# Kernel optimization log

Hardware: AMD Instinct MI355X
Metric: run time of the kernel (lower is better)

## Reference

```python
import jax, jax.numpy as jnp
import numpy as np

B, L, K, G, C, S = 1024, 32, 8, 8, 128, 32
D_IN = 2 * L + K + S  # masked z (L) + mask (L) + target (K) + shared (S)
TAU = 1.0
EPS = 1e-5
NEG_INF = -1e9  # stands in for torch's -9e15 diagonal fill; sigmoid(-1e9)=0


def setup_inputs() -> dict:
    key = jax.random.key(0)
    ks = jax.random.split(key, 24)
    eye = jnp.eye(K, dtype=bool)
    kaiming = lambda k, shape: jax.random.uniform(k, shape, jnp.float32, -1.0, 1.0) * np.sqrt(6.0 / shape[-1])
    return {
        "z_sample": jax.random.normal(ks[0], (B, L), jnp.float32),
        "target": jax.random.randint(ks[1], (B,), 0, K),
        "z_mean": jax.random.normal(ks[2], (B, L), jnp.float32),
        "z_logstd": 0.1 * jax.random.normal(ks[3], (B, L), jnp.float32),
        "z_shared": jax.random.normal(ks[4], (B, S), jnp.float32),
        "u_gumbel": jax.random.uniform(ks[5], (B, L, K), jnp.float32),
        "u_adj": jax.random.uniform(ks[6], (B, G, K, K), jnp.float32),
        "target_params": 0.1 * jax.random.normal(ks[7], (L, K), jnp.float32),
        "enco_theta": jnp.where(eye, NEG_INF, jax.random.normal(ks[8], (K, K), jnp.float32)),
        "enco_gamma": jnp.where(eye, NEG_INF, jax.random.normal(ks[9], (K, K), jnp.float32)),
        "W1": kaiming(ks[10], (L, C, D_IN)),
        "b1": jnp.zeros((L, C), jnp.float32),
        "gn1_w": jnp.ones((L, C), jnp.float32),
        "gn1_b": jnp.zeros((L, C), jnp.float32),
        "W2": kaiming(ks[11], (L, C, C)),
        "b2": jnp.zeros((L, C), jnp.float32),
        "gn2_w": jnp.ones((L, C), jnp.float32),
        "gn2_b": jnp.zeros((L, C), jnp.float32),
        "W3": 0.01 * jax.random.normal(ks[12], (L, 2, C), jnp.float32),
        "b3": jnp.zeros((L, 2), jnp.float32),
        "tanh_scale": jnp.zeros((L, 2), jnp.float32),
    }


def _mv_linear(x, W, b):
    # x: [B,G,L,d_in], W: [L,d_out,d_in] -> [B,G,L,d_out]  (per-latent independent linear)
    return jnp.einsum("bgld,lhd->bglh", x, W) + b


def _mv_groupnorm(x, w, b):
    # GroupNorm(L groups over L*C channels) == per-(sample, latent) normalization over C
    mu = x.mean(-1, keepdims=True)
    var = ((x - mu) ** 2).mean(-1, keepdims=True)
    return (x - mu) * jax.lax.rsqrt(var + EPS) * w + b


def reference(z_sample, target, z_mean, z_logstd, z_shared, u_gumbel, u_adj,
              target_params, enco_theta, enco_gamma,
              W1, b1, gn1_w, gn1_b, W2, b2, gn2_w, gn2_b, W3, b3, tanh_scale):
    dt = z_sample.dtype
    target_oh = jax.nn.one_hot(target, K, dtype=dt)  # [B,K]

    # hard gumbel-softmax with straight-through estimator: psi assigns latents to causal vars
    g = -jnp.log(-jnp.log(u_gumbel + 1e-10) + 1e-10)
    soft = jax.nn.softmax((target_params[None] + g) / TAU, axis=-1)  # [B,L,K]
    hard = jax.nn.one_hot(jnp.argmax(soft, axis=-1), K, dtype=dt)
    psi = hard + soft - jax.lax.stop_gradient(soft)  # [B,L,K]

    # ENCO graph sampling: edge prob = sigmoid(theta)*sigmoid(gamma), Bernoulli samples
    edge_prob = jax.nn.sigmoid(enco_theta) * jax.nn.sigmoid(enco_gamma)  # [K,K]
    adj = (u_adj < edge_prob[None, None]).astype(dt)  # [B,G,K,K], adj[k,l]=1: k->l

    # latent-level parent mask: mask[b,g,i,j]=1 iff latent j is a parent of latent i
    latent_mask = jnp.einsum("bil,bgkl,bjk->bgij", psi, adj, psi)  # [B,G,L,L]
    latent_mask = latent_mask * (1.0 - jnp.eye(L, dtype=dt))

    # per-latent network input: [masked parents, mask, intervention indicator, shared]
    z_masked = latent_mask * z_sample[:, None, None, :]                        # [B,G,L,L]
    t_inp = jnp.broadcast_to((psi * target_oh[:, None, :])[:, None], (B, G, L, K))
    zs = jnp.broadcast_to(z_shared[:, None, None, :], (B, G, L, S))
    s_inp = jnp.concatenate([z_masked, latent_mask, t_inp, zs], axis=-1)       # [B,G,L,D_IN]

    h = jax.nn.silu(_mv_groupnorm(_mv_linear(s_inp, W1, b1), gn1_w, gn1_b))
    h = jax.nn.silu(_mv_groupnorm(_mv_linear(h, W2, b2), gn2_w, gn2_b))
    h = _mv_linear(h, W3, b3)                                                  # [B,G,L,2]
    sc = jnp.exp(tanh_scale)                                                   # [L,2]
    h = jnp.tanh(h / sc) * sc                                                  # MultivarStableTanh
    prior_mean, prior_logstd = h[..., 0], h[..., 1]                            # [B,G,L]

    # KL(q(z) || p(z)) per latent, averaged over graph samples, summed over latents
    var_q = jnp.exp(2.0 * z_logstd)[:, None]                                   # [B,1,L]
    kld = (prior_logstd - z_logstd[:, None]
           + (var_q + (z_mean[:, None] - prior_mean) ** 2) / (2.0 * jnp.exp(2.0 * prior_logstd))
           - 0.5)                                                              # [B,G,L]
    return kld.mean(axis=1).sum(axis=-1)                                       # [B]
```

## Files before the change

kernel.cpp:

```cpp
#include <hip/hip_runtime.h>
#include <hip/hip_bf16.h>

#define B_DIM 1024
#define L_DIM 32
#define K_DIM 8
#define G_DIM 8
#define C_DIM 128
#define S_DIM 32
#define DIN   104

typedef __bf16  bf16x8 __attribute__((ext_vector_type(8)));
typedef float   f32x4  __attribute__((ext_vector_type(4)));
typedef float   f32x2  __attribute__((ext_vector_type(2)));

union frag_u { uint4 u; bf16x8 v; };

static __device__ __forceinline__ unsigned int pk2(float a, float b) {
    __hip_bfloat162 h = __float22bfloat162_rn(make_float2(a, b));
    union { __hip_bfloat162 h; unsigned int u; } v; v.h = h; return v.u;
}
static __device__ __forceinline__ unsigned int pk2v(f32x2 a) { return pk2(a.x, a.y); }
static __device__ __forceinline__ bf16x8 ld_frag(const unsigned short* p) {
    frag_u t; t.u = *(const uint4*)p; return t.v;
}

#define LOG2E 1.44269504f

__global__ __launch_bounds__(256) void prep_kernel(
    const float* __restrict__ u_gumbel,
    const float* __restrict__ u_adj,
    const float* __restrict__ target_params,
    const float* __restrict__ enco_theta,
    const float* __restrict__ enco_gamma,
    const int*   __restrict__ target,
    const float* __restrict__ W1,
    const float* __restrict__ W2,
    float*       __restrict__ out,
    unsigned char* __restrict__ cvarpk,
    unsigned int*  __restrict__ wsmask,
    unsigned short* __restrict__ wscr)
{
    const int t = threadIdx.x;
    if (blockIdx.x >= 1024) {
        int gtid  = (blockIdx.x - 1024) * 256 + t;
        int lane  = gtid & 63;
        int ks    = (gtid >> 6) & 3;
        int mt    = (gtid >> 8) & 3;
        int wm    = (gtid >> 10) & 1;
        int l     = (gtid >> 11) & 31;
        int which = gtid >> 16;
        int m  = 16 * (4 * wm + mt) + (lane & 15);
        int k0 = ks * 32 + (lane >> 4) * 8;
        uint4 o;
        if (which == 0) {
            if (k0 >= 104) {
                o = make_uint4(0u, 0u, 0u, 0u);
            } else {
                const float* p = W1 + (size_t)l * 13312 + m * 104 + k0;
                float4 a = *(const float4*)p, bq = *(const float4*)(p + 4);
                o = make_uint4(pk2(a.x, a.y), pk2(a.z, a.w), pk2(bq.x, bq.y), pk2(bq.z, bq.w));
            }
        } else {
            const float* p = W2 + (size_t)l * 16384 + m * 128 + k0;
            float4 a = *(const float4*)p, bq = *(const float4*)(p + 4);
            o = make_uint4(pk2(a.x, a.y), pk2(a.z, a.w), pk2(bq.x, bq.y), pk2(bq.z, bq.w));
        }
        *(uint4*)(wscr + (size_t)gtid * 8) = o;
        return;
    }

    __shared__ double ep[64];
    __shared__ unsigned char cv8[32];
    __shared__ unsigned long long adjb[8];
    const int b = blockIdx.x;
    if (t < 64) {
        double th = (double)enco_theta[t];
        double ga = (double)enco_gamma[t];
        ep[t] = (1.0 / (1.0 + exp(-th))) * (1.0 / (1.0 + exp(-ga)));
    }
    if (t == 0) out[b] = 0.0f;
    __syncthreads();

    {
        const int l = t >> 3, k = t & 7;
        float uf = u_gumbel[b * 256 + t];
        float gf = -__logf(-__logf(uf + 1e-10f) + 1e-10f);
        float vf = target_params[t] + gf;
        float vm = vf; int bk = k;
        #pragma unroll
        for (int off = 1; off < 8; off <<= 1) {
            float ov = __shfl_xor(vm, off, 64);
            int  obk = __shfl_xor(bk, off, 64);
            if (ov > vm || (ov == vm && obk < bk)) { vm = ov; bk = obk; }
        }
        int amb = ((k != bk) && (vm - vf < 1e-3f)) ? 1 : 0;
        #pragma unroll
        for (int off = 1; off < 8; off <<= 1) amb |= __shfl_xor(amb, off, 64);
        if (amb) {
            double ud = (double)uf;
            double gd = -log(-log(ud + 1e-10) + 1e-10);
            double vd = (double)target_params[t] + gd;
            int bk2 = k;
            #pragma unroll
            for (int off = 1; off < 8; off <<= 1) {
                double ov = __shfl_xor(vd, off, 64);
                int   obk = __shfl_xor(bk2, off, 64);
                if (ov > vd || (ov == vd && obk < bk2)) { vd = ov; bk2 = obk; }
            }
            bk = bk2;
        }
        if (k == 0) {
            int tg = target[b];
            unsigned char pkd = (unsigned char)(bk | ((bk == tg) ? 8 : 0));
            cvarpk[b * 32 + l] = pkd;
            cv8[l] = pkd;
        }
    }
    {
        const int wv = t >> 6, lane = t & 63;
        #pragma unroll
        for (int q = 0; q < 2; ++q) {
            int gg = wv + 4 * q;
            double u = (double)u_adj[b * 512 + gg * 64 + lane];
            unsigned long long m = __ballot(u < ep[lane]);
            if (lane == 0) adjb[gg] = m;
        }
    }
    __syncthreads();

    {
        const int g = t >> 5, l = t & 31;
        int lam = cv8[l] & 7;
        unsigned long long bits = adjb[g] >> lam;
        unsigned int mask = 0u;
        #pragma unroll
        for (int j = 0; j < 32; ++j) {
            int kap = cv8[j] & 7;
            mask |= ((unsigned int)(bits >> (kap * 8)) & 1u) << j;
        }
        mask &= ~(1u << l);
        wsmask[l * 8192 + b * 8 + g] = mask;
    }
}

__global__ __launch_bounds__(256, 2) void fused_kernel(
    const float* __restrict__ z_sample,
    const float* __restrict__ z_mean,
    const float* __restrict__ z_logstd,
    const float* __restrict__ z_shared,
    const float* __restrict__ pb1,
    const float* __restrict__ g1w,
    const float* __restrict__ g1b,
    const float* __restrict__ pb2,
    const float* __restrict__ g2w,
    const float* __restrict__ g2b,
    const float* __restrict__ W3,
    const float* __restrict__ pb3,
    const float* __restrict__ tsc,
    const unsigned short* __restrict__ wscr,
    const unsigned char*  __restrict__ cvarpk,
    const unsigned int*   __restrict__ wsmask,
    float* __restrict__ out)
{
    __shared__ __align__(16) unsigned short XH[4][32][136];
    __shared__ float p_g1w[128], p_g1b[128], p_b1[128];
    __shared__ float p_g2w[128], p_g2b[128], p_b2[128];
    __shared__ float p_w3[2][128];
    __shared__ float p_b3[2], p_ts[2];
    __shared__ unsigned int  msk[128];
    __shared__ unsigned char cvl[16];

    const int tid  = threadIdx.x;
    const int w    = tid >> 6, lane = tid & 63;
    const int lo   = lane & 15, hi = lane >> 4;
    const int l    = blockIdx.x & 31;
    const int grp  = blockIdx.x >> 5;

    if (tid < 128) {
        int c = tid;
        p_g1w[c] = g1w[l * 128 + c];  p_g1b[c] = g1b[l * 128 + c];
        p_b1[c]  = pb1[l * 128 + c];  p_w3[0][c] = W3[l * 256 + c];
        msk[c]   = wsmask[l * 8192 + grp * 128 + c];
    } else {
        int c = tid - 128;
        p_g2w[c] = g2w[l * 128 + c];  p_g2b[c] = g2b[l * 128 + c];
        p_b2[c]  = pb2[l * 128 + c];  p_w3[1][c] = W3[l * 256 + 128 + c];
    }
    if (tid < 16) cvl[tid] = cvarpk[(size_t)(grp * 16 + tid) * 32 + l];
    if (tid == 0) {
        p_b3[0] = pb3[l * 2];  p_b3[1] = pb3[l * 2 + 1];
        p_ts[0] = tsc[l * 2];  p_ts[1] = tsc[l * 2 + 1];
    }
    __syncthreads();

    #pragma unroll
    for (int nt = 0; nt < 2; ++nt) {
        int r  = nt * 16 + lo;
        int bl = (w * 32 + r) >> 3;
        int bg = grp * 16 + bl;
        unsigned int m32 = msk[w * 32 + r];
        unsigned int mq  = (m32 >> (hi * 8)) & 0xffu;
        const float4* zp = (const float4*)(z_sample + bg * 32 + hi * 8);
        float4 za = zp[0], zb = zp[1];
        uint4 f0;
        f0.x = pk2((mq & 1u)   ? za.x : 0.f, (mq & 2u)   ? za.y : 0.f);
        f0.y = pk2((mq & 4u)   ? za.z : 0.f, (mq & 8u)   ? za.w : 0.f);
        f0.z = pk2((mq & 16u)  ? zb.x : 0.f, (mq & 32u)  ? zb.y : 0.f);
        f0.w = pk2((mq & 64u)  ? zb.z : 0.f, (mq & 128u) ? zb.w : 0.f);
        uint4 f1;
        f1.x = ((mq & 1u)   ? 0x3F80u : 0u) | ((mq & 2u)   ? 0x3F800000u : 0u);
        f1.y = ((mq & 4u)   ? 0x3F80u : 0u) | ((mq & 8u)   ? 0x3F800000u : 0u);
        f1.z = ((mq & 16u)  ? 0x3F80u : 0u) | ((mq & 32u)  ? 0x3F800000u : 0u);
        f1.w = ((mq & 64u)  ? 0x3F80u : 0u) | ((mq & 128u) ? 0x3F800000u : 0u);
        unsigned int cb8 = cvl[bl];
        int lam = cb8 & 7, tf = (cb8 >> 3) & 1;
        int zsb = (hi == 0) ? 24 : (hi - 1) * 8;
        const float4* sp = (const float4*)(z_shared + bg * 32 + zsb);
        float4 sa = sp[0], sb = sp[1];
        uint4 fz;
        fz.x = pk2(sa.x, sa.y); fz.y = pk2(sa.z, sa.w);
        fz.z = pk2(sb.x, sb.y); fz.w = pk2(sb.z, sb.w);
        unsigned int ohw = tf ? (0x3F80u << ((lam & 1) << 4)) : 0u;
        int lq = lam >> 1;
        uint4 fo;
        fo.x = (lq == 0) ? ohw : 0u;
        fo.y = (lq == 1) ? ohw : 0u;
        fo.z = (lq == 2) ? ohw : 0u;
        fo.w = (lq == 3) ? ohw : 0u;
        bool h0 = (hi == 0);
        uint4 f2, f3;
        f2.x = h0 ? fo.x : fz.x;  f2.y = h0 ? fo.y : fz.y;
        f2.z = h0 ? fo.z : fz.z;  f2.w = h0 ? fo.w : fz.w;
        f3.x = h0 ? fz.x : 0u;    f3.y = h0 ? fz.y : 0u;
        f3.z = h0 ? fz.z : 0u;    f3.w = h0 ? fz.w : 0u;
        *(uint4*)&XH[w][r][hi * 8]      = f0;
        *(uint4*)&XH[w][r][32 + hi * 8] = f1;
        *(uint4*)&XH[w][r][64 + hi * 8] = f2;
        *(uint4*)&XH[w][r][96 + hi * 8] = f3;
    }

    const float inv128 = 1.0f / 128.0f;
    const unsigned short* w1p = wscr + (size_t)(l * 32) * 512 + lane * 8;
    const unsigned short* w2p = wscr + (size_t)((32 + l) * 32) * 512 + lane * 8;

    f32x4 acc[8][2];
    #pragma unroll
    for (int cb = 0; cb < 8; ++cb)
        #pragma unroll
        for (int nt = 0; nt < 2; ++nt) acc[cb][nt] = (f32x4){0.f, 0.f, 0.f, 0.f};
    {
        bf16x8 wfA[2], wfB[2];
        wfA[0] = ld_frag(w1p + 0 * 512);
        wfA[1] = ld_frag(w1p + 4 * 512);
        #pragma unroll
        for (int ks = 0; ks < 4; ++ks) {
            bf16x8 bf0 = ld_frag(&XH[w][lo][ks * 32 + hi * 8]);
            bf16x8 bf1 = ld_frag(&XH[w][16 + lo][ks * 32 + hi * 8]);
            #pragma unroll
            for (int p = 0; p < 4; ++p) {
                int ncb = (p < 3) ? (2 * p + 2) : 0;
                int nks = (p < 3) ? ks : ks + 1;
                if (p < 3 || ks < 3) {
                    wfB[0] = ld_frag(w1p + (ncb * 4 + nks) * 512);
                    wfB[1] = ld_frag(w1p + ((ncb + 1) * 4 + nks) * 512);
                }
                int cb = 2 * p;
                acc[cb][0]     = __builtin_amdgcn_mfma_f32_16x16x32_bf16(wfA[0], bf0, acc[cb][0], 0, 0, 0);
                acc[cb][1]     = __builtin_amdgcn_mfma_f32_16x16x32_bf16(wfA[0], bf1, acc[cb][1], 0, 0, 0);
                acc[cb + 1][0] = __builtin_amdgcn_mfma_f32_16x16x32_bf16(wfA[1], bf0, acc[cb + 1][0], 0, 0, 0);
                acc[cb + 1][1] = __builtin_amdgcn_mfma_f32_16x16x32_bf16(wfA[1], bf1, acc[cb + 1][1], 0, 0, 0);
                wfA[0] = wfB[0];  wfA[1] = wfB[1];
            }
        }
    }

    f32x2 s1v[2] = {(f32x2){0.f, 0.f}, (f32x2){0.f, 0.f}};
    f32x2 s2v[2] = {(f32x2){0.f, 0.f}, (f32x2){0.f, 0.f}};
    #pragma unroll
    for (int cb = 0; cb < 8; ++cb) {
        f32x2 bLo = *(const f32x2*)&p_b1[cb * 16 + hi * 4];
        f32x2 bHi = *(const f32x2*)&p_b1[cb * 16 + hi * 4 + 2];
        #pragma unroll
        for (int nt = 0; nt < 2; ++nt) {
            f32x2 vLo = (f32x2){acc[cb][nt][0], acc[cb][nt][1]} + bLo;
            f32x2 vHi = (f32x2){acc[cb][nt][2], acc[cb][nt][3]} + bHi;
            acc[cb][nt][0] = vLo.x;  acc[cb][nt][1] = vLo.y;
            acc[cb][nt][2] = vHi.x;  acc[cb][nt][3] = vHi.y;
            s1v[nt] += vLo + vHi;
            s2v[nt] += vLo * vLo + vHi * vHi;
        }
    }
    float rstd[2], nrm_off[2];
    #pragma unroll
    for (int nt = 0; nt < 2; ++nt) {
        float s1 = s1v[nt].x + s1v[nt].y;
        float s2 = s2v[nt].x + s2v[nt].y;
        s1 += __shfl_xor(s1, 16, 64);  s1 += __shfl_xor(s1, 32, 64);
        s2 += __shfl_xor(s2, 16, 64);  s2 += __shfl_xor(s2, 32, 64);
        float m_  = s1 * inv128;
        float var = s2 * inv128 - m_ * m_;
        float r   = rsqrtf(var + 1e-5f);
        rstd[nt] = r;  nrm_off[nt] = -m_ * r;
    }
    #pragma unroll
    for (int cb = 0; cb < 8; ++cb) {
        f32x2 gwLo = *(const f32x2*)&p_g1w[cb * 16 + hi * 4];
        f32x2 gwHi = *(const f32x2*)&p_g1w[cb * 16 + hi * 4 + 2];
        f32x2 gbLo = *(const f32x2*)&p_g1b[cb * 16 + hi * 4];
        f32x2 gbHi = *(const f32x2*)&p_g1b[cb * 16 + hi * 4 + 2];
        #pragma unroll
        for (int nt = 0; nt < 2; ++nt) {
            f32x2 rr  = (f32x2){rstd[nt], rstd[nt]};
            f32x2 oo  = (f32x2){nrm_off[nt], nrm_off[nt]};
            f32x2 vLo = (f32x2){acc[cb][nt][0], acc[cb][nt][1]};
            f32x2 vHi = (f32x2){acc[cb][nt][2], acc[cb][nt][3]};
            f32x2 xLo = (vLo * rr + oo) * gwLo + gbLo;
            f32x2 xHi = (vHi * rr + oo) * gwHi + gbHi;
            f32x2 aLo = xLo * (f32x2){-LOG2E, -LOG2E};
            f32x2 aHi = xHi * (f32x2){-LOG2E, -LOG2E};
            f32x2 eLo = (f32x2){__builtin_amdgcn_exp2f(aLo.x), __builtin_amdgcn_exp2f(aLo.y)};
            f32x2 eHi = (f32x2){__builtin_amdgcn_exp2f(aHi.x), __builtin_amdgcn_exp2f(aHi.y)};
            f32x2 dLo = eLo + (f32x2){1.f, 1.f};
            f32x2 dHi = eHi + (f32x2){1.f, 1.f};
            f32x2 yLo = xLo * (f32x2){__builtin_amdgcn_rcpf(dLo.x), __builtin_amdgcn_rcpf(dLo.y)};
            f32x2 yHi = xHi * (f32x2){__builtin_amdgcn_rcpf(dHi.x), __builtin_amdgcn_rcpf(dHi.y)};
            *(uint2*)&XH[w][nt * 16 + lo][cb * 16 + hi * 4] =
                make_uint2(pk2v(yLo), pk2v(yHi));
        }
    }

    #pragma unroll
    for (int cb = 0; cb < 8; ++cb)
        #pragma unroll
        for (int nt = 0; nt < 2; ++nt) acc[cb][nt] = (f32x4){0.f, 0.f, 0.f, 0.f};
    {
        bf16x8 wfA[2], wfB[2];
        wfA[0] = ld_frag(w2p + 0 * 512);
        wfA[1] = ld_frag(w2p + 4 * 512);
        #pragma unroll
        for (int ks = 0; ks < 4; ++ks) {
            bf16x8 bf0 = ld_frag(&XH[w][lo][ks * 32 + hi * 8]);
            bf16x8 bf1 = ld_frag(&XH[w][16 + lo][ks * 32 + hi * 8]);
            #pragma unroll
            for (int p = 0; p < 4; ++p) {
                int ncb = (p < 3) ? (2 * p + 2) : 0;
                int nks = (p < 3) ? ks : ks + 1;
                if (p < 3 || ks < 3) {
                    wfB[0] = ld_frag(w2p + (ncb * 4 + nks) * 512);
                    wfB[1] = ld_frag(w2p + ((ncb + 1) * 4 + nks) * 512);
                }
                int cb = 2 * p;
                acc[cb][0]     = __builtin_amdgcn_mfma_f32_16x16x32_bf16(wfA[0], bf0, acc[cb][0], 0, 0, 0);
                acc[cb][1]     = __builtin_amdgcn_mfma_f32_16x16x32_bf16(wfA[0], bf1, acc[cb][1], 0, 0, 0);
                acc[cb + 1][0] = __builtin_amdgcn_mfma_f32_16x16x32_bf16(wfA[1], bf0, acc[cb + 1][0], 0, 0, 0);
                acc[cb + 1][1] = __builtin_amdgcn_mfma_f32_16x16x32_bf16(wfA[1], bf1, acc[cb + 1][1], 0, 0, 0);
                wfA[0] = wfB[0];  wfA[1] = wfB[1];
            }
        }
    }

    f32x2 t1v[2] = {(f32x2){0.f, 0.f}, (f32x2){0.f, 0.f}};
    f32x2 t2v[2] = {(f32x2){0.f, 0.f}, (f32x2){0.f, 0.f}};
    #pragma unroll
    for (int cb = 0; cb < 8; ++cb) {
        f32x2 bLo = *(const f32x2*)&p_b2[cb * 16 + hi * 4];
        f32x2 bHi = *(const f32x2*)&p_b2[cb * 16 + hi * 4 + 2];
        #pragma unroll
        for (int nt = 0; nt < 2; ++nt) {
            f32x2 vLo = (f32x2){acc[cb][nt][0], acc[cb][nt][1]} + bLo;
            f32x2 vHi = (f32x2){acc[cb][nt][2], acc[cb][nt][3]} + bHi;
            acc[cb][nt][0] = vLo.x;  acc[cb][nt][1] = vLo.y;
            acc[cb][nt][2] = vHi.x;  acc[cb][nt][3] = vHi.y;
            t1v[nt] += vLo + vHi;
            t2v[nt] += vLo * vLo + vHi * vHi;
        }
    }
    float rstd2[2], off2[2];
    #pragma unroll
    for (int nt = 0; nt < 2; ++nt) {
        float s1 = t1v[nt].x + t1v[nt].y;
        float s2 = t2v[nt].x + t2v[nt].y;
        s1 += __shfl_xor(s1, 16, 64);  s1 += __shfl_xor(s1, 32, 64);
        s2 += __shfl_xor(s2, 16, 64);  s2 += __shfl_xor(s2, 32, 64);
        float m_  = s1 * inv128;
        float var = s2 * inv128 - m_ * m_;
        float r   = rsqrtf(var + 1e-5f);
        rstd2[nt] = r;  off2[nt] = -m_ * r;
    }
    f32x2 pm2[2] = {(f32x2){0.f, 0.f}, (f32x2){0.f, 0.f}};
    f32x2 pl2[2] = {(f32x2){0.f, 0.f}, (f32x2){0.f, 0.f}};
    #pragma unroll
    for (int cb = 0; cb < 8; ++cb) {
        f32x2 gwLo = *(const f32x2*)&p_g2w[cb * 16 + hi * 4];
        f32x2 gwHi = *(const f32x2*)&p_g2w[cb * 16 + hi * 4 + 2];
        f32x2 gbLo = *(const f32x2*)&p_g2b[cb * 16 + hi * 4];
        f32x2 gbHi = *(const f32x2*)&p_g2b[cb * 16 + hi * 4 + 2];
        f32x2 w0Lo = *(const f32x2*)&p_w3[0][cb * 16 + hi * 4];
        f32x2 w0Hi = *(const f32x2*)&p_w3[0][cb * 16 + hi * 4 + 2];
        f32x2 w1Lo = *(const f32x2*)&p_w3[1][cb * 16 + hi * 4];
        f32x2 w1Hi = *(const f32x2*)&p_w3[1][cb * 16 + hi * 4 + 2];
        #pragma unroll
        for (int nt = 0; nt < 2; ++nt) {
            f32x2 rr  = (f32x2){rstd2[nt], rstd2[nt]};
            f32x2 oo  = (f32x2){off2[nt], off2[nt]};
            f32x2 vLo = (f32x2){acc[cb][nt][0], acc[cb][nt][1]};
            f32x2 vHi = (f32x2){acc[cb][nt][2], acc[cb][nt][3]};
            f32x2 xLo = (vLo * rr + oo) * gwLo + gbLo;
            f32x2 xHi = (vHi * rr + oo) * gwHi + gbHi;
            f32x2 aLo = xLo * (f32x2){-LOG2E, -LOG2E};
            f32x2 aHi = xHi * (f32x2){-LOG2E, -LOG2E};
            f32x2 eLo = (f32x2){__builtin_amdgcn_exp2f(aLo.x), __builtin_amdgcn_exp2f(aLo.y)};
            f32x2 eHi = (f32x2){__builtin_amdgcn_exp2f(aHi.x), __builtin_amdgcn_exp2f(aHi.y)};
            f32x2 dLo = eLo + (f32x2){1.f, 1.f};
            f32x2 dHi = eHi + (f32x2){1.f, 1.f};
            f32x2 yLo = xLo * (f32x2){__builtin_amdgcn_rcpf(dLo.x), __builtin_amdgcn_rcpf(dLo.y)};
            f32x2 yHi = xHi * (f32x2){__builtin_amdgcn_rcpf(dHi.x), __builtin_amdgcn_rcpf(dHi.y)};
            pm2[nt] += yLo * w0Lo + yHi * w0Hi;
            pl2[nt] += yLo * w1Lo + yHi * w1Hi;
        }
    }

    {
        float sc0 = __expf(p_ts[0]), sc1 = __expf(p_ts[1]);
        float is0 = __expf(-p_ts[0]), is1 = __expf(-p_ts[1]);
        #pragma unroll
        for (int nt = 0; nt < 2; ++nt) {
            int r  = w * 32 + nt * 16 + lo;
            int bg = grp * 16 + (r >> 3);
            float zm = z_mean[bg * 32 + l];
            float zl = z_logstd[bg * 32 + l];
            float pmp = pm2[nt].x + pm2[nt].y;
            float plp = pl2[nt].x + pl2[nt].y;
            pmp += __shfl_xor(pmp, 16, 64);  pmp += __shfl_xor(pmp, 32, 64);
            plp += __shfl_xor(plp, 16, 64);  plp += __shfl_xor(plp, 32, 64);
            float pm = pmp + p_b3[0];
            float pl = plp + p_b3[1];
            float e0 = __expf(2.0f * pm * is0);
            pm = (1.0f - 2.0f * __fdividef(1.0f, e0 + 1.0f)) * sc0;
            float e1 = __expf(2.0f * pl * is1);
            pl = (1.0f - 2.0f * __fdividef(1.0f, e1 + 1.0f)) * sc1;
            float vq = __expf(2.0f * zl);
            float d  = zm - pm;
            float kld = pl - zl + (vq + d * d) * 0.5f * __expf(-2.0f * pl) - 0.5f;
            kld += __shfl_xor(kld, 1, 64);
            kld += __shfl_xor(kld, 2, 64);
            kld += __shfl_xor(kld, 4, 64);
            if (hi == 0 && (lo & 7) == 0) atomicAdd(&out[bg], kld * 0.125f);
        }
    }
}

extern "C" void kernel_launch(void* const* d_in, const int* in_sizes, int n_in,
                              void* d_out, int out_size, void* d_ws, size_t ws_size,
                              hipStream_t stream) {
    const float* z_sample      = (const float*)d_in[0];
    const int*   target        = (const int*)d_in[1];
    const float* z_mean        = (const float*)d_in[2];
    const float* z_logstd      = (const float*)d_in[3];
    const float* z_shared      = (const float*)d_in[4];
    const float* u_gumbel      = (const float*)d_in[5];
    const float* u_adj         = (const float*)d_in[6];
    const float* target_params = (const float*)d_in[7];
    const float* enco_theta    = (const float*)d_in[8];
    const float* enco_gamma    = (const float*)d_in[9];
    const float* W1            = (const float*)d_in[10];
    const float* pb1           = (const float*)d_in[11];
    const float* g1w           = (const float*)d_in[12];
    const float* g1b           = (const float*)d_in[13];
    const float* W2            = (const float*)d_in[14];
    const float* pb2           = (const float*)d_in[15];
    const float* g2w           = (const float*)d_in[16];
    const float* g2b           = (const float*)d_in[17];
    const float* W3            = (const float*)d_in[18];
    const float* pb3           = (const float*)d_in[19];
    const float* tsc           = (const float*)d_in[20];

    unsigned char* cvarpk = (unsigned char*)d_ws;
    unsigned int*  wsmask = (unsigned int*)((char*)d_ws + 32768);
    unsigned short* wscr  = (unsigned short*)((char*)d_ws + 32768 + 1048576);

    prep_kernel<<<1536, 256, 0, stream>>>(u_gumbel, u_adj, target_params,
                                          enco_theta, enco_gamma, target,
                                          W1, W2, (float*)d_out,
                                          cvarpk, wsmask, wscr);
    fused_kernel<<<2048, 256, 0, stream>>>(z_sample, z_mean, z_logstd, z_shared,
                                           pb1, g1w, g1b, pb2, g2w, g2b,
                                           W3, pb3, tsc, wscr, cvarpk, wsmask,
                                           (float*)d_out);
}
```

Before: 156.9 us.

## Split fused kernel into single-wave blocks and drop block barrier

Changes the fused kernel from 4-wave blocks to 1-wave blocks with 4x more blocks, each handling 4 batch rows for one latent. Each block now loads its own per-latent norm/bias parameters, removing the __syncthreads and shrinking LDS per block. This trades extra redundant parameter loads for finer-grained scheduling and no barrier.

```diff
diff --git a/kernel.cpp b/kernel.cpp
--- a/kernel.cpp
+++ b/kernel.cpp
@@ -143,7 +143,7 @@
     }
 }
 
-__global__ __launch_bounds__(256, 2) void fused_kernel(
+__global__ __launch_bounds__(64, 2) void fused_kernel(
     const float* __restrict__ z_sample,
     const float* __restrict__ z_mean,
     const float* __restrict__ z_logstd,
@@ -162,43 +162,40 @@
     const unsigned int*   __restrict__ wsmask,
     float* __restrict__ out)
 {
-    __shared__ __align__(16) unsigned short XH[4][32][136];
+    __shared__ __align__(16) unsigned short XH[32][136];
     __shared__ float p_g1w[128], p_g1b[128], p_b1[128];
     __shared__ float p_g2w[128], p_g2b[128], p_b2[128];
     __shared__ float p_w3[2][128];
     __shared__ float p_b3[2], p_ts[2];
-    __shared__ unsigned int  msk[128];
-    __shared__ unsigned char cvl[16];
-
-    const int tid  = threadIdx.x;
-    const int w    = tid >> 6, lane = tid & 63;
+    __shared__ unsigned int  msk[32];
+    __shared__ unsigned char cvl[4];
+
+    const int lane = threadIdx.x & 63;
     const int lo   = lane & 15, hi = lane >> 4;
     const int l    = blockIdx.x & 31;
     const int grp  = blockIdx.x >> 5;
 
-    if (tid < 128) {
-        int c = tid;
+    #pragma unroll
+    for (int j = 0; j < 2; ++j) {
+        int c = lane + j * 64;
         p_g1w[c] = g1w[l * 128 + c];  p_g1b[c] = g1b[l * 128 + c];
         p_b1[c]  = pb1[l * 128 + c];  p_w3[0][c] = W3[l * 256 + c];
-        msk[c]   = wsmask[l * 8192 + grp * 128 + c];
-    } else {
-        int c = tid - 128;
         p_g2w[c] = g2w[l * 128 + c];  p_g2b[c] = g2b[l * 128 + c];
         p_b2[c]  = pb2[l * 128 + c];  p_w3[1][c] = W3[l * 256 + 128 + c];
     }
-    if (tid < 16) cvl[tid] = cvarpk[(size_t)(grp * 16 + tid) * 32 + l];
-    if (tid == 0) {
+    if (lane < 32) msk[lane] = wsmask[l * 8192 + grp * 32 + lane];
+    if (lane < 4)  cvl[lane] = cvarpk[(size_t)(grp * 4 + lane) * 32 + l];
+    if (lane == 0) {
         p_b3[0] = pb3[l * 2];  p_b3[1] = pb3[l * 2 + 1];
         p_ts[0] = tsc[l * 2];  p_ts[1] = tsc[l * 2 + 1];
     }
-    __syncthreads();
 
     #pragma unroll
     for (int nt = 0; nt < 2; ++nt) {
         int r  = nt * 16 + lo;
-        int bl = (w * 32 + r) >> 3;
-        int bg = grp * 16 + bl;
-        unsigned int m32 = msk[w * 32 + r];
+        int bl = r >> 3;
+        int bg = grp * 4 + bl;
+        unsigned int m32 = msk[r];
         unsigned int mq  = (m32 >> (hi * 8)) & 0xffu;
         const float4* zp = (const float4*)(z_sample + bg * 32 + hi * 8);
         float4 za = zp[0], zb = zp[1];
@@ -233,10 +230,10 @@
         f2.z = h0 ? fo.z : fz.z;  f2.w = h0 ? fo.w : fz.w;
         f3.x = h0 ? fz.x : 0u;    f3.y = h0 ? fz.y : 0u;
         f3.z = h0 ? fz.z : 0u;    f3.w = h0 ? fz.w : 0u;
-        *(uint4*)&XH[w][r][hi * 8]      = f0;
-        *(uint4*)&XH[w][r][32 + hi * 8] = f1;
-        *(uint4*)&XH[w][r][64 + hi * 8] = f2;
-        *(uint4*)&XH[w][r][96 + hi * 8] = f3;
+        *(uint4*)&XH[r][hi * 8]      = f0;
+        *(uint4*)&XH[r][32 + hi * 8] = f1;
+        *(uint4*)&XH[r][64 + hi * 8] = f2;
+        *(uint4*)&XH[r][96 + hi * 8] = f3;
     }
 
     const float inv128 = 1.0f / 128.0f;
@@ -254,8 +251,8 @@
         wfA[1] = ld_frag(w1p + 4 * 512);
         #pragma unroll
         for (int ks = 0; ks < 4; ++ks) {
-            bf16x8 bf0 = ld_frag(&XH[w][lo][ks * 32 + hi * 8]);
-            bf16x8 bf1 = ld_frag(&XH[w][16 + lo][ks * 32 + hi * 8]);
+            bf16x8 bf0 = ld_frag(&XH[lo][ks * 32 + hi * 8]);
+            bf16x8 bf1 = ld_frag(&XH[16 + lo][ks * 32 + hi * 8]);
             #pragma unroll
             for (int p = 0; p < 4; ++p) {
                 int ncb = (p < 3) ? (2 * p + 2) : 0;
@@ -324,7 +321,7 @@
             f32x2 dHi = eHi + (f32x2){1.f, 1.f};
             f32x2 yLo = xLo * (f32x2){__builtin_amdgcn_rcpf(dLo.x), __builtin_amdgcn_rcpf(dLo.y)};
             f32x2 yHi = xHi * (f32x2){__builtin_amdgcn_rcpf(dHi.x), __builtin_amdgcn_rcpf(dHi.y)};
-            *(uint2*)&XH[w][nt * 16 + lo][cb * 16 + hi * 4] =
+            *(uint2*)&XH[nt * 16 + lo][cb * 16 + hi * 4] =
                 make_uint2(pk2v(yLo), pk2v(yHi));
         }
     }
@@ -339,8 +336,8 @@
         wfA[1] = ld_frag(w2p + 4 * 512);
         #pragma unroll
         for (int ks = 0; ks < 4; ++ks) {
-            bf16x8 bf0 = ld_frag(&XH[w][lo][ks * 32 + hi * 8]);
-            bf16x8 bf1 = ld_frag(&XH[w][16 + lo][ks * 32 + hi * 8]);
+            bf16x8 bf0 = ld_frag(&XH[lo][ks * 32 + hi * 8]);
+            bf16x8 bf1 = ld_frag(&XH[16 + lo][ks * 32 + hi * 8]);
             #pragma unroll
             for (int p = 0; p < 4; ++p) {
                 int ncb = (p < 3) ? (2 * p + 2) : 0;
@@ -425,8 +422,8 @@
         float is0 = __expf(-p_ts[0]), is1 = __expf(-p_ts[1]);
         #pragma unroll
         for (int nt = 0; nt < 2; ++nt) {
-            int r  = w * 32 + nt * 16 + lo;
-            int bg = grp * 16 + (r >> 3);
+            int r  = nt * 16 + lo;
+            int bg = grp * 4 + (r >> 3);
             float zm = z_mean[bg * 32 + l];
             float zl = z_logstd[bg * 32 + l];
             float pmp = pm2[nt].x + pm2[nt].y;
@@ -483,8 +480,8 @@
                                           enco_theta, enco_gamma, target,
                                           W1, W2, (float*)d_out,
                                           cvarpk, wsmask, wscr);
-    fused_kernel<<<2048, 256, 0, stream>>>(z_sample, z_mean, z_logstd, z_shared,
-                                           pb1, g1w, g1b, pb2, g2w, g2b,
-                                           W3, pb3, tsc, wscr, cvarpk, wsmask,
-                                           (float*)d_out);
+    fused_kernel<<<8192, 64, 0, stream>>>(z_sample, z_mean, z_logstd, z_shared,
+                                          pb1, g1w, g1b, pb2, g2w, g2b,
+                                          W3, pb3, tsc, wscr, cvarpk, wsmask,
+                                          (float*)d_out);
 }
```

New measurement: 159.3 us. Within noise of the previous version (+1.5%).
